# Kernel optimization log

Measured on AMD Instinct MI355X. Metric: run time of the kernel, lower is better.

The kernel has to match this reference:

```python
import jax, jax.numpy as jnp
import numpy as np

N_NODES = 100000
N_EDGES = 1_600_000
IN_CH = 64
HID = 128
OUT_CH = 2


def _glorot(key, shape):
    fan_in = shape[0]
    return jax.random.normal(key, shape, dtype=jnp.float32) / jnp.sqrt(jnp.float32(fan_in))


def setup_inputs() -> dict:
    key = jax.random.key(0)
    ks = jax.random.split(key, 10)
    x = jax.random.normal(ks[0], (N_NODES, IN_CH), dtype=jnp.float32)
    edge_index = jax.random.randint(ks[1], (2, N_EDGES), 0, N_NODES, dtype=jnp.int64)
    # SAGEConv layer 0: lin_l (neighbor, with bias) + lin_r (root)
    W_n0 = _glorot(ks[2], (IN_CH, HID))
    W_s0 = _glorot(ks[3], (IN_CH, HID))
    b0 = jnp.zeros((HID,), dtype=jnp.float32)
    # SAGEConv layer 1
    W_n1 = _glorot(ks[4], (HID, HID))
    W_s1 = _glorot(ks[5], (HID, HID))
    b1 = jnp.zeros((HID,), dtype=jnp.float32)
    # final fc
    fc_w = _glorot(ks[6], (HID, OUT_CH))
    fc_b = jnp.zeros((OUT_CH,), dtype=jnp.float32)
    return {"x": x, "edge_index": edge_index, "W_n0": W_n0, "W_s0": W_s0, "b0": b0,
            "W_n1": W_n1, "W_s1": W_s1, "b1": b1, "fc_w": fc_w, "fc_b": fc_b}


def _sage_conv(h, src, dst, W_n, W_s, b, num_nodes):
    # mean aggregation of source features onto destination nodes
    agg = jax.ops.segment_sum(h[src], dst, num_segments=num_nodes)  # [N, d]
    cnt = jax.ops.segment_sum(jnp.ones_like(dst, dtype=h.dtype), dst, num_segments=num_nodes)
    mean = agg / jnp.maximum(cnt, 1.0)[:, None]
    return mean @ W_n + h @ W_s + b


def reference(x, edge_index, W_n0, W_s0, b0, W_n1, W_s1, b1, fc_w, fc_b):
    src, dst = edge_index[0], edge_index[1]
    n = x.shape[0]
    h = jax.nn.relu(_sage_conv(x, src, dst, W_n0, W_s0, b0, n))  # dropout is identity in eval mode
    h = jax.nn.relu(_sage_conv(h, src, dst, W_n1, W_s1, b1, n))
    return h @ fc_w + fc_b
```

## Files before the change

### kernel.cpp

```cpp
#include <hip/hip_runtime.h>

#define N_NODES 100000
#define IN_CH 64
#define HID 128
#define NBUCK ((N_NODES + 511) >> 9)
#define NCB 256

typedef short short8 __attribute__((ext_vector_type(8)));
typedef float floatx4 __attribute__((ext_vector_type(4)));
typedef float floatx2 __attribute__((ext_vector_type(2)));

__device__ __forceinline__ unsigned short f2bf(float f) {
    unsigned u = __builtin_bit_cast(unsigned, f);
    u += 0x7fffu + ((u >> 16) & 1u);
    return (unsigned short)(u >> 16);
}

template <int K>
__device__ __forceinline__ void pack_dev(const float* __restrict__ Wn,
                                         const float* __restrict__ Ws,
                                         unsigned short* __restrict__ Bpack, int idx) {
    int s = idx >> 9;
    int rem = idx & 511;
    int t = rem >> 6;
    int lane = rem & 63;
    int quad = lane >> 4;
    int n = t * 16 + (lane & 15);
    unsigned short v[8];
#pragma unroll
    for (int j = 0; j < 8; ++j) {
        int k = s * 32 + quad * 8 + j;
        float w = (k < K) ? Wn[(size_t)k * HID + n] : Ws[(size_t)(k - K) * HID + n];
        v[j] = f2bf(w);
    }
    *(short8*)(Bpack + (size_t)idx * 8) = *(short8*)v;
}

__global__ __launch_bounds__(256) void histprep_kernel(const int* __restrict__ dst,
                                                       int* __restrict__ table, int E, int chunk,
                                                       const float* __restrict__ x,
                                                       unsigned short* __restrict__ x_bf,
                                                       unsigned char* __restrict__ x_f8,
                                                       const float* __restrict__ Wn0,
                                                       const float* __restrict__ Ws0,
                                                       unsigned short* __restrict__ Bpack0,
                                                       const float* __restrict__ Wn1,
                                                       const float* __restrict__ Ws1,
                                                       unsigned short* __restrict__ Bpack1,
                                                       int* __restrict__ scan_done, int n4) {
    int b = blockIdx.x;
    if (b < NCB) {
        if (b == 0 && threadIdx.x == 0) *scan_done = 0;
        __shared__ int h[NBUCK];
        for (int i = threadIdx.x; i < NBUCK; i += 256) h[i] = 0;
        __syncthreads();
        int e0 = b * chunk;
        int e1 = min(E, e0 + chunk);
        for (int e = e0 + threadIdx.x; e < e1; e += 256) atomicAdd(&h[dst[e] >> 9], 1);
        __syncthreads();
        for (int i = threadIdx.x; i < NBUCK; i += 256) table[i * NCB + b] = h[i];
    } else if (b < NCB + 8) {
        pack_dev<IN_CH>(Wn0, Ws0, Bpack0, (b - NCB) * 256 + threadIdx.x);
    } else if (b < NCB + 24) {
        pack_dev<HID>(Wn1, Ws1, Bpack1, (b - NCB - 8) * 256 + threadIdx.x);
    } else {
        int i = (b - NCB - 24) * 256 + threadIdx.x;
        if (i < n4) {
            float4 v = ((const float4*)x)[i];
            ushort4 o;
            o.x = f2bf(v.x); o.y = f2bf(v.y); o.z = f2bf(v.z); o.w = f2bf(v.w);
            ((ushort4*)x_bf)[i] = o;
            int p8 = __builtin_amdgcn_cvt_pk_fp8_f32(v.x, v.y, 0, false);
            p8 = __builtin_amdgcn_cvt_pk_fp8_f32(v.z, v.w, p8, true);
            ((unsigned*)x_f8)[i] = (unsigned)p8;
        }
    }
}

__global__ __launch_bounds__(256) void scan12_kernel(int* __restrict__ table,
                                                     int* __restrict__ tot,
                                                     int* __restrict__ bstart,
                                                     int* __restrict__ ptr,
                                                     int* __restrict__ scan_done, int E) {
    __shared__ int s[NCB];
    __shared__ int lastflag;
    int b = blockIdx.x, t = threadIdx.x;
    int c = table[b * NCB + t];
    s[t] = c;
    __syncthreads();
#pragma unroll
    for (int off = 1; off < NCB; off <<= 1) {
        int v = (t >= off) ? s[t - off] : 0;
        __syncthreads();
        s[t] += v;
        __syncthreads();
    }
    table[b * NCB + t] = s[t] - c;
    if (t == NCB - 1) {
        __hip_atomic_store(&tot[b], s[t], __ATOMIC_RELAXED, __HIP_MEMORY_SCOPE_AGENT);
        int prev = __hip_atomic_fetch_add(scan_done, 1, __ATOMIC_ACQ_REL, __HIP_MEMORY_SCOPE_AGENT);
        lastflag = (prev == NBUCK - 1);
    }
    __syncthreads();
    if (!lastflag) return;
    int v = (t < NBUCK) ? __hip_atomic_load(&tot[t], __ATOMIC_RELAXED, __HIP_MEMORY_SCOPE_AGENT) : 0;
    s[t] = v;
    __syncthreads();
#pragma unroll
    for (int off = 1; off < 256; off <<= 1) {
        int u = (t >= off) ? s[t - off] : 0;
        __syncthreads();
        s[t] += u;
        __syncthreads();
    }
    if (t < NBUCK) bstart[t] = s[t] - v;
    if (t == 0) {
        bstart[NBUCK] = E;
        ptr[N_NODES] = E;
    }
}

__global__ __launch_bounds__(256) void bin_kernel(const int* __restrict__ src,
                                                  const int* __restrict__ dst,
                                                  const int* __restrict__ table,
                                                  const int* __restrict__ bstart,
                                                  unsigned* __restrict__ binned, int E, int chunk) {
    __shared__ int cur[NBUCK];
    int blk = blockIdx.x;
    for (int i = threadIdx.x; i < NBUCK; i += 256) cur[i] = bstart[i] + table[i * NCB + blk];
    __syncthreads();
    int e0 = blk * chunk;
    int e1 = min(E, e0 + chunk);
    for (int e = e0 + threadIdx.x; e < e1; e += 256) {
        int d = dst[e];
        int b = d >> 9;
        int pos = atomicAdd(&cur[b], 1);
        if ((unsigned)pos < (unsigned)E)
            binned[pos] = (unsigned)src[e] | ((unsigned)(d & 511) << 17);
    }
}

__global__ __launch_bounds__(256) void place_kernel(const unsigned* __restrict__ binned,
                                                    const int* __restrict__ bstart,
                                                    int* __restrict__ ptr,
                                                    int* __restrict__ sorted, int N, int E) {
    __shared__ int deg[512];
    __shared__ int cur[512];
    __shared__ int ssum[256];
    int b = blockIdx.x, t = threadIdx.x;
    int start = bstart[b], end = bstart[b + 1];
    start = max(0, min(start, E));
    end = max(start, min(end, E));
    deg[t] = 0;
    deg[t + 256] = 0;
    __syncthreads();
    for (int i = start + t; i < end; i += 256) atomicAdd(&deg[(binned[i] >> 17) & 511], 1);
    __syncthreads();
    int a = deg[2 * t], c = deg[2 * t + 1];
    int s2 = a + c;
    ssum[t] = s2;
    __syncthreads();
#pragma unroll
    for (int off = 1; off < 256; off <<= 1) {
        int u = (t >= off) ? ssum[t - off] : 0;
        __syncthreads();
        ssum[t] += u;
        __syncthreads();
    }
    int excl2 = ssum[t] - s2;
    cur[2 * t] = excl2;
    cur[2 * t + 1] = excl2 + a;
    int n0 = b * 512 + 2 * t;
    if (n0 < N) ptr[n0] = start + excl2;
    if (n0 + 1 < N) ptr[n0 + 1] = start + excl2 + a;
    __syncthreads();
    for (int i = start + t; i < end; i += 256) {
        unsigned p = binned[i];
        int dl = (p >> 17) & 511;
        int pos = start + atomicAdd(&cur[dl], 1);
        if ((unsigned)pos < (unsigned)E) sorted[pos] = (int)(p & 0x1FFFF);
    }
}

template <int C>
__global__ __launch_bounds__(256) void gather_mean_f8(const int* __restrict__ ptr,
                                                      const int* __restrict__ srcs,
                                                      const unsigned char* __restrict__ feat,
                                                      unsigned short* __restrict__ mean, int N,
                                                      int E) {
    constexpr int NA = C / 64;
    int w = (blockIdx.x * blockDim.x + threadIdx.x) >> 6;
    if (w >= N) return;
    int lane = threadIdx.x & 63;
    int g = lane >> 4;
    int l = lane & 15;
    int s0 = ptr[w], s1 = ptr[w + 1];
    s0 = max(0, min(s0, E));
    s1 = max(s0, min(s1, E));
    int deg = min(s1 - s0, 4096);

    floatx2 acc2[2 * NA];
#pragma unroll
    for (int u = 0; u < 2 * NA; ++u) { acc2[u][0] = 0.0f; acc2[u][1] = 0.0f; }

    for (int jb = 0; jb < deg; jb += 64) {
        int rem = min(64, deg - jb);
        int idxreg = (jb + lane < deg) ? srcs[s0 + jb + lane] : 0;
        int fullend = rem & ~15;
        int o0 = 0;
        for (; o0 < fullend; o0 += 16) {
            uint v[4][NA];
#pragma unroll
            for (int q = 0; q < 4; ++q) {
                int idx = (int)min((unsigned)__shfl(idxreg, o0 + q * 4 + g),
                                   (unsigned)(N_NODES - 1));
                if (NA == 2) {
                    uint2 tt = *(const uint2*)(feat + (size_t)idx * C + l * 8);
                    v[q][0] = tt.x; v[q][1] = tt.y;
                } else {
                    v[q][0] = *(const unsigned*)(feat + (size_t)idx * C + l * 4);
                }
            }
#pragma unroll
            for (int q = 0; q < 4; ++q)
#pragma unroll
                for (int a = 0; a < NA; ++a) {
                    acc2[2 * a + 0] += __builtin_amdgcn_cvt_pk_f32_fp8(v[q][a], false);
                    acc2[2 * a + 1] += __builtin_amdgcn_cvt_pk_f32_fp8(v[q][a], true);
                }
        }
        if (o0 < rem) {
            uint v[4][NA];
#pragma unroll
            for (int q = 0; q < 4; ++q) {
                int o = o0 + q * 4 + g;
                int idx = (int)min((unsigned)__shfl(idxreg, o), (unsigned)(N_NODES - 1));
#pragma unroll
                for (int a = 0; a < NA; ++a) v[q][a] = 0;
                if (o < rem) {
                    if (NA == 2) {
                        uint2 tt = *(const uint2*)(feat + (size_t)idx * C + l * 8);
                        v[q][0] = tt.x; v[q][1] = tt.y;
                    } else {
                        v[q][0] = *(const unsigned*)(feat + (size_t)idx * C + l * 4);
                    }
                }
            }
#pragma unroll
            for (int q = 0; q < 4; ++q)
#pragma unroll
                for (int a = 0; a < NA; ++a) {
                    acc2[2 * a + 0] += __builtin_amdgcn_cvt_pk_f32_fp8(v[q][a], false);
                    acc2[2 * a + 1] += __builtin_amdgcn_cvt_pk_f32_fp8(v[q][a], true);
                }
        }
    }
#pragma unroll
    for (int m = 16; m < 64; m <<= 1) {
#pragma unroll
        for (int u = 0; u < 2 * NA; ++u) {
            acc2[u][0] += __shfl_xor(acc2[u][0], m, 64);
            acc2[u][1] += __shfl_xor(acc2[u][1], m, 64);
        }
    }
    if (g == 0) {
        float inv = (deg > 0) ? 1.0f / (float)deg : 0.0f;
        unsigned short o[4 * NA];
#pragma unroll
        for (int u = 0; u < 2 * NA; ++u) {
            o[2 * u + 0] = f2bf(acc2[u][0] * inv);
            o[2 * u + 1] = f2bf(acc2[u][1] * inv);
        }
        if (NA == 2) *(uint4*)(mean + (size_t)w * C + l * 8) = *(const uint4*)o;
        else *(uint2*)(mean + (size_t)w * C + l * 4) = *(const uint2*)o;
    }
}

template <int KT, bool FUSE_FC>
__global__ __launch_bounds__(256) void sage_gemm_mfma(const unsigned short* __restrict__ meanb,
                                                      const unsigned short* __restrict__ hb,
                                                      const unsigned short* __restrict__ Bpack,
                                                      const float* __restrict__ bias,
                                                      const float* __restrict__ fcw,
                                                      const float* __restrict__ fcb,
                                                      unsigned short* __restrict__ outb,
                                                      unsigned char* __restrict__ out8,
                                                      float* __restrict__ outf, int N) {
    constexpr int KH = KT / 2;
    constexpr int LDA = KT + 8;
    __shared__ unsigned short As[64 * LDA];
    const int t = threadIdx.x;
    const int row0 = blockIdx.x * 64;

    constexpr int SEGS = KT / 8;
    for (int c = t; c < 64 * SEGS; c += 256) {
        int r = c / SEGS, seg = c % SEGS;
        int rsrc = row0 + r;
        if (rsrc >= N) rsrc = N - 1;
        const unsigned short* srcp = (seg < SEGS / 2)
                                         ? meanb + (size_t)rsrc * KH + seg * 8
                                         : hb + (size_t)rsrc * KH + (seg - SEGS / 2) * 8;
        *(uint4*)&As[r * LDA + seg * 8] = *(const uint4*)srcp;
    }
    __syncthreads();

    const int lane = t & 63;
    const int wave = t >> 6;
    const int quad = lane >> 4;
    const int lo = lane & 15;

    floatx4 acc[8];
#pragma unroll
    for (int i = 0; i < 8; ++i)
#pragma unroll
        for (int r = 0; r < 4; ++r) acc[i][r] = 0.0f;

    const unsigned short* abase = &As[(wave * 16 + lo) * LDA + quad * 8];
#pragma unroll
    for (int s = 0; s < KT / 32; ++s) {
        short8 a = *(const short8*)(abase + s * 32);
        const short8* bp = (const short8*)Bpack + (size_t)(s * 8) * 64 + lane;
#pragma unroll
        for (int tt = 0; tt < 8; ++tt) {
            short8 b = bp[tt * 64];
            acc[tt] = __builtin_amdgcn_mfma_f32_16x16x32_bf16(a, b, acc[tt], 0, 0, 0);
        }
    }

    if (!FUSE_FC) {
        __syncthreads();
#pragma unroll
        for (int tt = 0; tt < 8; ++tt) {
            int col = tt * 16 + lo;
            float bv = bias[col];
#pragma unroll
            for (int r = 0; r < 4; ++r) {
                int rl = wave * 16 + quad * 4 + r;
                As[rl * LDA + col] = f2bf(fmaxf(acc[tt][r] + bv, 0.0f));
            }
        }
        __syncthreads();
        for (int i = t; i < 64 * (HID / 8); i += 256) {
            int r = i >> 4, ch = i & 15;
            int row = row0 + r;
            if (row < N)
                *(uint4*)(outb + (size_t)row * HID + ch * 8) = *(const uint4*)&As[r * LDA + ch * 8];
        }
        __syncthreads();
        unsigned char* As8 = (unsigned char*)As;
#pragma unroll
        for (int tt = 0; tt < 8; ++tt) {
            int col = tt * 16 + lo;
            float bv = bias[col];
#pragma unroll
            for (int r = 0; r < 4; ++r) {
                int rl = wave * 16 + quad * 4 + r;
                float v = fmaxf(acc[tt][r] + bv, 0.0f);
                int p8 = __builtin_amdgcn_cvt_pk_fp8_f32(v, v, 0, false);
                As8[rl * (LDA * 2) + col] = (unsigned char)(p8 & 0xff);
            }
        }
        __syncthreads();
        for (int i = t; i < 64 * (HID / 16); i += 256) {
            int r = i >> 3, ch = i & 7;
            int row = row0 + r;
            if (row < N)
                *(uint4*)(out8 + (size_t)row * HID + ch * 16) =
                    *(const uint4*)&As8[r * (LDA * 2) + ch * 16];
        }
    } else {
        float o0[4] = {}, o1[4] = {};
#pragma unroll
        for (int tt = 0; tt < 8; ++tt) {
            int col = tt * 16 + lo;
            float bv = bias[col];
            float w0 = fcw[col * 2 + 0];
            float w1 = fcw[col * 2 + 1];
#pragma unroll
            for (int r = 0; r < 4; ++r) {
                float v = fmaxf(acc[tt][r] + bv, 0.0f);
                o0[r] += v * w0;
                o1[r] += v * w1;
            }
        }
#pragma unroll
        for (int r = 0; r < 4; ++r) {
#pragma unroll
            for (int m = 8; m >= 1; m >>= 1) {
                o0[r] += __shfl_xor(o0[r], m, 16);
                o1[r] += __shfl_xor(o1[r], m, 16);
            }
        }
        if (lo == 0) {
#pragma unroll
            for (int r = 0; r < 4; ++r) {
                int row = row0 + wave * 16 + quad * 4 + r;
                if (row < N) {
                    outf[(size_t)row * 2 + 0] = o0[r] + fcb[0];
                    outf[(size_t)row * 2 + 1] = o1[r] + fcb[1];
                }
            }
        }
    }
}

extern "C" void kernel_launch(void* const* d_in, const int* in_sizes, int n_in,
                              void* d_out, int out_size, void* d_ws, size_t ws_size,
                              hipStream_t stream) {
    const float* x   = (const float*)d_in[0];
    const int*   ei  = (const int*)d_in[1];
    const float* Wn0 = (const float*)d_in[2];
    const float* Ws0 = (const float*)d_in[3];
    const float* b0  = (const float*)d_in[4];
    const float* Wn1 = (const float*)d_in[5];
    const float* Ws1 = (const float*)d_in[6];
    const float* b1  = (const float*)d_in[7];
    const float* fcw = (const float*)d_in[8];
    const float* fcb = (const float*)d_in[9];
    float* out = (float*)d_out;

    const int E = in_sizes[1] / 2;
    const int* src = ei;
    const int* dst = ei + E;
    const int N = N_NODES;
    const int chunk = (E + NCB - 1) / NCB;

    char* ws = (char*)d_ws;
    size_t off = 0;
    int* table  = (int*)(ws + off); off += (size_t)NBUCK * NCB * 4;
    int* tot    = (int*)(ws + off); off += 4096;
    int* bstart = (int*)(ws + off); off += 4096;
    int* scan_done = (int*)(ws + off); off += 256;
    int* ptr    = (int*)(ws + off); off += (size_t)(N + 1) * 4 + 60; off &= ~(size_t)63;
    unsigned* binned = (unsigned*)(ws + off); off += (size_t)E * 4;
    int* sorted = (int*)(ws + off); off += (size_t)E * 4;
    off = (off + 255) & ~(size_t)255;
    unsigned short* x_bf   = (unsigned short*)(ws + off); off += (size_t)N * IN_CH * 2;
    unsigned short* mean0  = (unsigned short*)(ws + off); off += (size_t)N * IN_CH * 2;
    unsigned short* h1_bf  = (unsigned short*)(ws + off); off += (size_t)N * HID * 2;
    unsigned short* mean1  = (unsigned short*)(ws + off); off += (size_t)N * HID * 2;
    unsigned char*  h1_f8  = (unsigned char*)(ws + off);  off += (size_t)N * HID;
    unsigned char*  x_f8   = (unsigned char*)(ws + off);  off += (size_t)N * IN_CH;
    off = (off + 255) & ~(size_t)255;
    unsigned short* Bpack0 = (unsigned short*)(ws + off); off += (size_t)(2 * IN_CH / 32) * 8 * 64 * 8 * 2;
    unsigned short* Bpack1 = (unsigned short*)(ws + off); off += (size_t)(2 * HID / 32) * 8 * 64 * 8 * 2;

    {
        int n4 = N * IN_CH / 4;
        int nblk = NCB + 24 + (n4 + 255) / 256;
        histprep_kernel<<<nblk, 256, 0, stream>>>(dst, table, E, chunk, x, x_bf, x_f8,
                                                  Wn0, Ws0, Bpack0, Wn1, Ws1, Bpack1,
                                                  scan_done, n4);
    }
    scan12_kernel<<<NBUCK, 256, 0, stream>>>(table, tot, bstart, ptr, scan_done, E);
    bin_kernel<<<NCB, 256, 0, stream>>>(src, dst, table, bstart, binned, E, chunk);
    place_kernel<<<NBUCK, 256, 0, stream>>>(binned, bstart, ptr, sorted, N, E);

    gather_mean_f8<IN_CH><<<(N * 64 + 255) / 256, 256, 0, stream>>>(ptr, sorted, x_f8, mean0, N, E);
    sage_gemm_mfma<2 * IN_CH, false><<<(N + 63) / 64, 256, 0, stream>>>(
        mean0, x_bf, Bpack0, b0, nullptr, nullptr, h1_bf, h1_f8, nullptr, N);

    gather_mean_f8<HID><<<(N * 64 + 255) / 256, 256, 0, stream>>>(ptr, sorted, h1_f8, mean1, N, E);
    sage_gemm_mfma<2 * HID, true><<<(N + 63) / 64, 256, 0, stream>>>(
        mean1, h1_bf, Bpack1, b1, fcw, fcb, nullptr, nullptr, out, N);
}
```

Measured before the change: 254.3 us.

## Assign one 16-lane group per node in gather-mean instead of one wavefront

The gather-mean kernel now maps each 16-lane quarter-wave to its own destination node, so one wavefront processes four nodes, where before a whole wavefront handled one node. Each group loads neighbor indices directly with broadcast loads, keeps four independent accumulators, and drops the cross-group shuffle reduction and the shuffle-based index distribution. This targets the wasted lanes and reduction overhead on low-degree nodes (average degree about 16). In exchange, degree imbalance between the four nodes sharing a wave causes divergence, and the per-edge index loads are redundant across lanes.

```diff
diff --git a/kernel.cpp b/kernel.cpp
--- a/kernel.cpp
+++ b/kernel.cpp
@@ -183,97 +183,97 @@
 }
 
 template <int C>
-__global__ __launch_bounds__(256) void gather_mean_f8(const int* __restrict__ ptr,
+__global__ __launch_bounds__(256) void gather_mean_g4(const int* __restrict__ ptr,
                                                       const int* __restrict__ srcs,
                                                       const unsigned char* __restrict__ feat,
                                                       unsigned short* __restrict__ mean, int N,
                                                       int E) {
     constexpr int NA = C / 64;
-    int w = (blockIdx.x * blockDim.x + threadIdx.x) >> 6;
+    const int lane = threadIdx.x & 63;
+    const int g = lane >> 4;
+    const int l = lane & 15;
+    const int w = (blockIdx.x * 4 + (threadIdx.x >> 6)) * 4 + g;
     if (w >= N) return;
-    int lane = threadIdx.x & 63;
-    int g = lane >> 4;
-    int l = lane & 15;
     int s0 = ptr[w], s1 = ptr[w + 1];
     s0 = max(0, min(s0, E));
     s1 = max(s0, min(s1, E));
-    int deg = min(s1 - s0, 4096);
-
-    floatx2 acc2[2 * NA];
-#pragma unroll
-    for (int u = 0; u < 2 * NA; ++u) { acc2[u][0] = 0.0f; acc2[u][1] = 0.0f; }
-
-    for (int jb = 0; jb < deg; jb += 64) {
-        int rem = min(64, deg - jb);
-        int idxreg = (jb + lane < deg) ? srcs[s0 + jb + lane] : 0;
-        int fullend = rem & ~15;
-        int o0 = 0;
-        for (; o0 < fullend; o0 += 16) {
-            uint v[4][NA];
-#pragma unroll
-            for (int q = 0; q < 4; ++q) {
-                int idx = (int)min((unsigned)__shfl(idxreg, o0 + q * 4 + g),
-                                   (unsigned)(N_NODES - 1));
-                if (NA == 2) {
-                    uint2 tt = *(const uint2*)(feat + (size_t)idx * C + l * 8);
-                    v[q][0] = tt.x; v[q][1] = tt.y;
-                } else {
-                    v[q][0] = *(const unsigned*)(feat + (size_t)idx * C + l * 4);
-                }
-            }
-#pragma unroll
-            for (int q = 0; q < 4; ++q)
-#pragma unroll
-                for (int a = 0; a < NA; ++a) {
-                    acc2[2 * a + 0] += __builtin_amdgcn_cvt_pk_f32_fp8(v[q][a], false);
-                    acc2[2 * a + 1] += __builtin_amdgcn_cvt_pk_f32_fp8(v[q][a], true);
-                }
-        }
-        if (o0 < rem) {
-            uint v[4][NA];
-#pragma unroll
-            for (int q = 0; q < 4; ++q) {
-                int o = o0 + q * 4 + g;
-                int idx = (int)min((unsigned)__shfl(idxreg, o), (unsigned)(N_NODES - 1));
-#pragma unroll
-                for (int a = 0; a < NA; ++a) v[q][a] = 0;
-                if (o < rem) {
-                    if (NA == 2) {
-                        uint2 tt = *(const uint2*)(feat + (size_t)idx * C + l * 8);
-                        v[q][0] = tt.x; v[q][1] = tt.y;
-                    } else {
-                        v[q][0] = *(const unsigned*)(feat + (size_t)idx * C + l * 4);
-                    }
-                }
-            }
-#pragma unroll
-            for (int q = 0; q < 4; ++q)
-#pragma unroll
-                for (int a = 0; a < NA; ++a) {
-                    acc2[2 * a + 0] += __builtin_amdgcn_cvt_pk_f32_fp8(v[q][a], false);
-                    acc2[2 * a + 1] += __builtin_amdgcn_cvt_pk_f32_fp8(v[q][a], true);
-                }
-        }
-    }
-#pragma unroll
-    for (int m = 16; m < 64; m <<= 1) {
-#pragma unroll
-        for (int u = 0; u < 2 * NA; ++u) {
-            acc2[u][0] += __shfl_xor(acc2[u][0], m, 64);
-            acc2[u][1] += __shfl_xor(acc2[u][1], m, 64);
-        }
-    }
-    if (g == 0) {
-        float inv = (deg > 0) ? 1.0f / (float)deg : 0.0f;
-        unsigned short o[4 * NA];
-#pragma unroll
-        for (int u = 0; u < 2 * NA; ++u) {
-            o[2 * u + 0] = f2bf(acc2[u][0] * inv);
-            o[2 * u + 1] = f2bf(acc2[u][1] * inv);
-        }
-        if (NA == 2) *(uint4*)(mean + (size_t)w * C + l * 8) = *(const uint4*)o;
-        else *(uint2*)(mean + (size_t)w * C + l * 4) = *(const uint2*)o;
-    }
+    const int deg = min(s1 - s0, 4096);
+
+    floatx2 accq[4][2 * NA];
+#pragma unroll
+    for (int q = 0; q < 4; ++q)
+#pragma unroll
+        for (int u = 0; u < 2 * NA; ++u) { accq[q][u][0] = 0.0f; accq[q][u][1] = 0.0f; }
+
+    const int nfull = deg & ~3;
+    int j = 0;
+    for (; j < nfull; j += 4) {
+        int cid[4];
+#pragma unroll
+        for (int q = 0; q < 4; ++q)
+            cid[q] = (int)min((unsigned)srcs[s0 + j + q], (unsigned)(N_NODES - 1));
+        uint v[4][NA];
+#pragma unroll
+        for (int q = 0; q < 4; ++q) {
+            if (NA == 2) {
+                uint2 tt = *(const uint2*)(feat + (size_t)cid[q] * C + l * 8);
+                v[q][0] = tt.x; v[q][1] = tt.y;
+            } else {
+                v[q][0] = *(const unsigned*)(feat + (size_t)cid[q] * C + l * 4);
+            }
+        }
+#pragma unroll
+        for (int q = 0; q < 4; ++q)
+#pragma unroll
+            for (int a = 0; a < NA; ++a) {
+                accq[q][2 * a + 0] += __builtin_amdgcn_cvt_pk_f32_fp8(v[q][a], false);
+                accq[q][2 * a + 1] += __builtin_amdgcn_cvt_pk_f32_fp8(v[q][a], true);
+            }
+    }
+    if (j < deg) {
+        int cid[4];
+#pragma unroll
+        for (int q = 0; q < 4; ++q) {
+            int jj = min(j + q, deg - 1);
+            cid[q] = (int)min((unsigned)srcs[s0 + jj], (unsigned)(N_NODES - 1));
+        }
+        uint v[4][NA];
+#pragma unroll
+        for (int q = 0; q < 4; ++q) {
+            if (NA == 2) {
+                uint2 tt = *(const uint2*)(feat + (size_t)cid[q] * C + l * 8);
+                v[q][0] = tt.x; v[q][1] = tt.y;
+            } else {
+                v[q][0] = *(const unsigned*)(feat + (size_t)cid[q] * C + l * 4);
+            }
+        }
+#pragma unroll
+        for (int q = 0; q < 4; ++q)
+#pragma unroll
+            for (int a = 0; a < NA; ++a) v[q][a] = (j + q < deg) ? v[q][a] : 0u;
+#pragma unroll
+        for (int q = 0; q < 4; ++q)
+#pragma unroll
+            for (int a = 0; a < NA; ++a) {
+                accq[q][2 * a + 0] += __builtin_amdgcn_cvt_pk_f32_fp8(v[q][a], false);
+                accq[q][2 * a + 1] += __builtin_amdgcn_cvt_pk_f32_fp8(v[q][a], true);
+            }
+    }
+#pragma unroll
+    for (int u = 0; u < 2 * NA; ++u) {
+        accq[0][u] += accq[1][u];
+        accq[2][u] += accq[3][u];
+        accq[0][u] += accq[2][u];
+    }
+    const float inv = (deg > 0) ? 1.0f / (float)deg : 0.0f;
+    unsigned short o[4 * NA];
+#pragma unroll
+    for (int u = 0; u < 2 * NA; ++u) {
+        o[2 * u + 0] = f2bf(accq[0][u][0] * inv);
+        o[2 * u + 1] = f2bf(accq[0][u][1] * inv);
+    }
+    if (NA == 2) *(uint4*)(mean + (size_t)w * C + l * 8) = *(const uint4*)o;
+    else *(uint2*)(mean + (size_t)w * C + l * 4) = *(const uint2*)o;
 }
 
 template <int KT, bool FUSE_FC>
@@ -456,11 +456,12 @@
     bin_kernel<<<NCB, 256, 0, stream>>>(src, dst, table, bstart, binned, E, chunk);
     place_kernel<<<NBUCK, 256, 0, stream>>>(binned, bstart, ptr, sorted, N, E);
 
-    gather_mean_f8<IN_CH><<<(N * 64 + 255) / 256, 256, 0, stream>>>(ptr, sorted, x_f8, mean0, N, E);
+    const int gblk = (N + 15) / 16;
+    gather_mean_g4<IN_CH><<<gblk, 256, 0, stream>>>(ptr, sorted, x_f8, mean0, N, E);
     sage_gemm_mfma<2 * IN_CH, false><<<(N + 63) / 64, 256, 0, stream>>>(
         mean0, x_bf, Bpack0, b0, nullptr, nullptr, h1_bf, h1_f8, nullptr, N);
 
-    gather_mean_f8<HID><<<(N * 64 + 255) / 256, 256, 0, stream>>>(ptr, sorted, h1_f8, mean1, N, E);
+    gather_mean_g4<HID><<<gblk, 256, 0, stream>>>(ptr, sorted, h1_f8, mean1, N, E);
     sage_gemm_mfma<2 * HID, true><<<(N + 63) / 64, 256, 0, stream>>>(
         mean1, h1_bf, Bpack1, b1, fcw, fcb, nullptr, nullptr, out, N);
 }
```

Measured after the change: 245.8 us. -3.3%, faster.
